# Performance work log

Hardware: AMD Instinct MI355X
Metric: run time of the kernel (lower is better)

Reference implementation:

```python
import jax, jax.numpy as jnp
import numpy as np

G, W, H1, H2, H3 = 512, 64, 128, 128, 64
B = 1024

def setup_inputs() -> dict:
    key = jax.random.key(0)
    k0, k1, k2, k3 = jax.random.split(key, 4)
    inputs = jax.random.normal(k0, (B, G * W), dtype=jnp.float32)
    # Glorot-uniform-like scaled init for stacked per-SKU weights
    def glorot(k, shape):
        fan_in, fan_out = shape[-2], shape[-1]
        lim = jnp.sqrt(6.0 / (fan_in + fan_out)).astype(jnp.float32)
        return jax.random.uniform(k, shape, jnp.float32, -lim, lim)
    W1 = glorot(k1, (G, W, H1))
    W2 = glorot(k2, (G, H1, H2))
    W3 = glorot(k3, (G, H2, H3))
    return {"inputs": inputs, "W1": W1, "W2": W2, "W3": W3}

def reference(inputs, W1, W2, W3):
    # inputs: [B, G*W]  -> per-SKU blocks [B, G, W] (SKU-major slicing in original)
    b = inputs.shape[0]
    x = inputs.reshape(b, G, W)
    # Grouped (batched-over-SKU) GEMM + relu per layer; no dropout (training=None)
    x = jax.nn.relu(jnp.einsum('bgw,gwh->bgh', x, W1))  # [B, G, H1]
    x = jax.nn.relu(jnp.einsum('bgh,ghk->bgk', x, W2))  # [B, G, H2]
    x = jax.nn.relu(jnp.einsum('bgk,gko->bgo', x, W3))  # [B, G, H3]
    # concat of per-SKU outputs along axis 1 == SKU-major reshape
    return x.reshape(b, G * H3)
```

## Files before the change

### kernel.cpp

```cpp
#include <hip/hip_runtime.h>

#define NG  512
#define WIN 64
#define NH1 128
#define NH2 128
#define NH3 64
#define NBB 1024
#define GW  (NG*WIN)
#define GH3 (NG*NH3)

typedef __attribute__((ext_vector_type(8))) short bf16x8;
typedef __attribute__((ext_vector_type(4))) float f32x4;
typedef __attribute__((ext_vector_type(4))) unsigned int u32x4;

union frag_u { u32x4 u; bf16x8 h; };

__device__ __forceinline__ unsigned pk2bf(float a, float b) {
  unsigned ua = __builtin_bit_cast(unsigned, a);
  unsigned ub = __builtin_bit_cast(unsigned, b);
  ua += 0x7fffu + ((ua >> 16) & 1u);
  ub += 0x7fffu + ((ub >> 16) & 1u);
  return (ua >> 16) | (ub & 0xffff0000u);
}

__device__ __forceinline__ void permswap(unsigned &e, unsigned &o) {
  asm volatile("s_nop 1\n\t"
               "v_permlane32_swap_b32 %0, %1\n\t"
               "s_nop 1\n\t"
               "v_permlane16_swap_b32 %0, %1\n\t"
               "s_nop 1"
               : "+v"(e), "+v"(o));
}

template<int K, int H>
__device__ __forceinline__ void stage_frag(const float* __restrict__ gsrc,
                                           char* ldsBase, int tid) {
  constexpr int KC = K / 32;
  constexpr int NELEM = (K / 8) * H;
  #pragma unroll
  for (int lin = tid; lin < NELEM; lin += 512) {
    const int h  = lin & (H - 1);
    const int kb = lin / H;
    const float* p = gsrc + h + (size_t)(8 * kb) * H;
    unsigned w0 = pk2bf(p[0 * H], p[1 * H]);
    unsigned w1 = pk2bf(p[2 * H], p[3 * H]);
    unsigned w2 = pk2bf(p[4 * H], p[5 * H]);
    unsigned w3 = pk2bf(p[6 * H], p[7 * H]);
    const int mt = h >> 4, bl = h & 15, kc = kb >> 2, bq = kb & 3;
    const int byteoff = ((mt * KC + kc) * 64 + bq * 16 + bl) * 16;
    *(u32x4*)(ldsBase + byteoff) = (u32x4){w0, w1, w2, w3};
  }
}

__device__ __forceinline__ void mk_bfrag(const f32x4* acc, frag_u* bf) {
  #pragma unroll
  for (int kc = 0; kc < 4; ++kc) {
    f32x4 e = acc[2 * kc], o = acc[2 * kc + 1];
    unsigned E0 = pk2bf(fmaxf(e[0], 0.f), fmaxf(e[1], 0.f));
    unsigned E1 = pk2bf(fmaxf(e[2], 0.f), fmaxf(e[3], 0.f));
    unsigned O0 = pk2bf(fmaxf(o[0], 0.f), fmaxf(o[1], 0.f));
    unsigned O1 = pk2bf(fmaxf(o[2], 0.f), fmaxf(o[3], 0.f));
    permswap(E0, O0);
    permswap(E1, O1);
    bf[kc].u = (u32x4){E0, E1, O0, O1};
  }
}

__device__ __forceinline__ void ld_b1(const float* px, frag_u* b1) {
  #pragma unroll
  for (int kc = 0; kc < 2; ++kc) {
    f32x4 lo = *(const f32x4*)(px + 32 * kc);
    f32x4 hi = *(const f32x4*)(px + 32 * kc + 4);
    b1[kc].u = (u32x4){pk2bf(lo[0], lo[1]), pk2bf(lo[2], lo[3]),
                       pk2bf(hi[0], hi[1]), pk2bf(hi[2], hi[3])};
  }
}

__global__ __launch_bounds__(512, 4)
void DeepBlockDense_kernel(const float* __restrict__ x,
                           const float* __restrict__ w1,
                           const float* __restrict__ w2,
                           const float* __restrict__ w3,
                           float* __restrict__ out) {
  __shared__ __align__(16) char smem[65536];
  const int g    = blockIdx.x;
  const int tid  = threadIdx.x;
  const int lane = tid & 63;
  const int wid  = tid >> 6;
  const int bq   = lane >> 4;
  const int bl   = lane & 15;

  stage_frag<64 , 128>(w1 + (size_t)g * (64 * 128) , smem        , tid);
  stage_frag<128, 128>(w2 + (size_t)g * (128 * 128), smem + 16384, tid);
  stage_frag<128, 64 >(w3 + (size_t)g * (128 * 64) , smem + 49152, tid);
  __syncthreads();

  const char* aBase = smem + lane * 16;

  #pragma unroll 1
  for (int t = 0; t < 4; ++t) {
    const size_t r0 = (size_t)(t * 256 + wid * 16 + bl);
    const size_t r1 = r0 + 128;

    frag_u b1a[2], b1b[2];
    ld_b1(x + r0 * GW + g * 64 + 8 * bq, b1a);
    ld_b1(x + r1 * GW + g * 64 + 8 * bq, b1b);

    f32x4 acc1a[8] = {}, acc1b[8] = {};
    #pragma unroll
    for (int mt = 0; mt < 8; ++mt) {
      #pragma unroll
      for (int kc = 0; kc < 2; ++kc) {
        frag_u a;
        a.u = *(const u32x4*)(aBase + 1024 * (mt * 2 + kc));
        acc1a[mt] = __builtin_amdgcn_mfma_f32_16x16x32_bf16(a.h, b1a[kc].h, acc1a[mt], 0, 0, 0);
        acc1b[mt] = __builtin_amdgcn_mfma_f32_16x16x32_bf16(a.h, b1b[kc].h, acc1b[mt], 0, 0, 0);
      }
    }

    frag_u b2a[4], b2b[4];
    mk_bfrag(acc1a, b2a);
    mk_bfrag(acc1b, b2b);

    f32x4 acc2a[8] = {}, acc2b[8] = {};
    #pragma unroll
    for (int mt = 0; mt < 8; ++mt) {
      #pragma unroll
      for (int kc = 0; kc < 4; ++kc) {
        frag_u a;
        a.u = *(const u32x4*)(aBase + 16384 + 1024 * (mt * 4 + kc));
        acc2a[mt] = __builtin_amdgcn_mfma_f32_16x16x32_bf16(a.h, b2a[kc].h, acc2a[mt], 0, 0, 0);
        acc2b[mt] = __builtin_amdgcn_mfma_f32_16x16x32_bf16(a.h, b2b[kc].h, acc2b[mt], 0, 0, 0);
      }
    }

    frag_u b3a[4], b3b[4];
    mk_bfrag(acc2a, b3a);
    mk_bfrag(acc2b, b3b);

    f32x4 acc3a[4] = {}, acc3b[4] = {};
    #pragma unroll
    for (int mt = 0; mt < 4; ++mt) {
      #pragma unroll
      for (int kc = 0; kc < 4; ++kc) {
        frag_u a;
        a.u = *(const u32x4*)(aBase + 49152 + 1024 * (mt * 4 + kc));
        acc3a[mt] = __builtin_amdgcn_mfma_f32_16x16x32_bf16(a.h, b3a[kc].h, acc3a[mt], 0, 0, 0);
        acc3b[mt] = __builtin_amdgcn_mfma_f32_16x16x32_bf16(a.h, b3b[kc].h, acc3b[mt], 0, 0, 0);
      }
    }

    float* po0 = out + r0 * GH3 + g * 64 + 4 * bq;
    float* po1 = out + r1 * GH3 + g * 64 + 4 * bq;
    #pragma unroll
    for (int mt = 0; mt < 4; ++mt) {
      f32x4 va = acc3a[mt], vb = acc3b[mt];
      va[0] = fmaxf(va[0], 0.f); va[1] = fmaxf(va[1], 0.f);
      va[2] = fmaxf(va[2], 0.f); va[3] = fmaxf(va[3], 0.f);
      vb[0] = fmaxf(vb[0], 0.f); vb[1] = fmaxf(vb[1], 0.f);
      vb[2] = fmaxf(vb[2], 0.f); vb[3] = fmaxf(vb[3], 0.f);
      *(f32x4*)(po0 + 16 * mt) = va;
      *(f32x4*)(po1 + 16 * mt) = vb;
    }
  }
}

extern "C" void kernel_launch(void* const* d_in, const int* in_sizes, int n_in,
                              void* d_out, int out_size, void* d_ws, size_t ws_size,
                              hipStream_t stream) {
  const float* x  = (const float*)d_in[0];
  const float* w1 = (const float*)d_in[1];
  const float* w2 = (const float*)d_in[2];
  const float* w3 = (const float*)d_in[3];
  float* out = (float*)d_out;
  (void)in_sizes; (void)n_in; (void)out_size; (void)d_ws; (void)ws_size;
  DeepBlockDense_kernel<<<dim3(NG), dim3(512), 0, stream>>>(x, w1, w2, w3, out);
}
```

Before: 87.54 us.

## Interleave layer GEMMs per output-tile pair and use hardware bf16 conversion

```diff
diff --git a/kernel.cpp b/kernel.cpp
--- a/kernel.cpp
+++ b/kernel.cpp
@@ -1,26 +1,21 @@
 #include <hip/hip_runtime.h>
 
 #define NG  512
-#define WIN 64
-#define NH1 128
-#define NH2 128
-#define NH3 64
-#define NBB 1024
-#define GW  (NG*WIN)
-#define GH3 (NG*NH3)
+#define GW  32768
+#define GH3 32768
 
 typedef __attribute__((ext_vector_type(8))) short bf16x8;
 typedef __attribute__((ext_vector_type(4))) float f32x4;
 typedef __attribute__((ext_vector_type(4))) unsigned int u32x4;
+typedef __attribute__((ext_vector_type(2))) __bf16 bf16x2;
 
 union frag_u { u32x4 u; bf16x8 h; };
 
-__device__ __forceinline__ unsigned pk2bf(float a, float b) {
-  unsigned ua = __builtin_bit_cast(unsigned, a);
-  unsigned ub = __builtin_bit_cast(unsigned, b);
-  ua += 0x7fffu + ((ua >> 16) & 1u);
-  ub += 0x7fffu + ((ub >> 16) & 1u);
-  return (ua >> 16) | (ub & 0xffff0000u);
+#define MFMA __builtin_amdgcn_mfma_f32_16x16x32_bf16
+
+__device__ __forceinline__ unsigned cvt2bf(float a, float b) {
+  bf16x2 v = {(__bf16)a, (__bf16)b};
+  return __builtin_bit_cast(unsigned, v);
 }
 
 __device__ __forceinline__ void permswap(unsigned &e, unsigned &o) {
@@ -30,6 +25,16 @@
                "v_permlane16_swap_b32 %0, %1\n\t"
                "s_nop 1"
                : "+v"(e), "+v"(o));
+}
+
+__device__ __forceinline__ void mk_bfrag1(f32x4 e, f32x4 o, frag_u &bf) {
+  unsigned E0 = cvt2bf(fmaxf(e[0], 0.f), fmaxf(e[1], 0.f));
+  unsigned E1 = cvt2bf(fmaxf(e[2], 0.f), fmaxf(e[3], 0.f));
+  unsigned O0 = cvt2bf(fmaxf(o[0], 0.f), fmaxf(o[1], 0.f));
+  unsigned O1 = cvt2bf(fmaxf(o[2], 0.f), fmaxf(o[3], 0.f));
+  permswap(E0, O0);
+  permswap(E1, O1);
+  bf.u = (u32x4){E0, E1, O0, O1};
 }
 
 template<int K, int H>
@@ -42,27 +47,13 @@
     const int h  = lin & (H - 1);
     const int kb = lin / H;
     const float* p = gsrc + h + (size_t)(8 * kb) * H;
-    unsigned w0 = pk2bf(p[0 * H], p[1 * H]);
-    unsigned w1 = pk2bf(p[2 * H], p[3 * H]);
-    unsigned w2 = pk2bf(p[4 * H], p[5 * H]);
-    unsigned w3 = pk2bf(p[6 * H], p[7 * H]);
+    unsigned w0 = cvt2bf(p[0 * H], p[1 * H]);
+    unsigned w1 = cvt2bf(p[2 * H], p[3 * H]);
+    unsigned w2 = cvt2bf(p[4 * H], p[5 * H]);
+    unsigned w3 = cvt2bf(p[6 * H], p[7 * H]);
     const int mt = h >> 4, bl = h & 15, kc = kb >> 2, bq = kb & 3;
     const int byteoff = ((mt * KC + kc) * 64 + bq * 16 + bl) * 16;
     *(u32x4*)(ldsBase + byteoff) = (u32x4){w0, w1, w2, w3};
-  }
-}
-
-__device__ __forceinline__ void mk_bfrag(const f32x4* acc, frag_u* bf) {
-  #pragma unroll
-  for (int kc = 0; kc < 4; ++kc) {
-    f32x4 e = acc[2 * kc], o = acc[2 * kc + 1];
-    unsigned E0 = pk2bf(fmaxf(e[0], 0.f), fmaxf(e[1], 0.f));
-    unsigned E1 = pk2bf(fmaxf(e[2], 0.f), fmaxf(e[3], 0.f));
-    unsigned O0 = pk2bf(fmaxf(o[0], 0.f), fmaxf(o[1], 0.f));
-    unsigned O1 = pk2bf(fmaxf(o[2], 0.f), fmaxf(o[3], 0.f));
-    permswap(E0, O0);
-    permswap(E1, O1);
-    bf[kc].u = (u32x4){E0, E1, O0, O1};
   }
 }
 
@@ -71,8 +62,8 @@
   for (int kc = 0; kc < 2; ++kc) {
     f32x4 lo = *(const f32x4*)(px + 32 * kc);
     f32x4 hi = *(const f32x4*)(px + 32 * kc + 4);
-    b1[kc].u = (u32x4){pk2bf(lo[0], lo[1]), pk2bf(lo[2], lo[3]),
-                       pk2bf(hi[0], hi[1]), pk2bf(hi[2], hi[3])};
+    b1[kc].u = (u32x4){cvt2bf(lo[0], lo[1]), cvt2bf(lo[2], lo[3]),
+                       cvt2bf(hi[0], hi[1]), cvt2bf(hi[2], hi[3])};
   }
 }
 
@@ -88,7 +79,6 @@
   const int lane = tid & 63;
   const int wid  = tid >> 6;
   const int bq   = lane >> 4;
-  const int bl   = lane & 15;
 
   stage_frag<64 , 128>(w1 + (size_t)g * (64 * 128) , smem        , tid);
   stage_frag<128, 128>(w2 + (size_t)g * (128 * 128), smem + 16384, tid);
@@ -99,54 +89,54 @@
 
   #pragma unroll 1
   for (int t = 0; t < 4; ++t) {
-    const size_t r0 = (size_t)(t * 256 + wid * 16 + bl);
+    const size_t r0 = (size_t)(t * 256 + wid * 16 + (lane & 15));
     const size_t r1 = r0 + 128;
 
     frag_u b1a[2], b1b[2];
     ld_b1(x + r0 * GW + g * 64 + 8 * bq, b1a);
     ld_b1(x + r1 * GW + g * 64 + 8 * bq, b1b);
 
-    f32x4 acc1a[8] = {}, acc1b[8] = {};
+    frag_u b2a[4], b2b[4];
     #pragma unroll
-    for (int mt = 0; mt < 8; ++mt) {
+    for (int pr = 0; pr < 4; ++pr) {
+      f32x4 ea = {}, oa = {}, eb = {}, ob = {};
       #pragma unroll
       for (int kc = 0; kc < 2; ++kc) {
-        frag_u a;
-        a.u = *(const u32x4*)(aBase + 1024 * (mt * 2 + kc));
-        acc1a[mt] = __builtin_amdgcn_mfma_f32_16x16x32_bf16(a.h, b1a[kc].h, acc1a[mt], 0, 0, 0);
-        acc1b[mt] = __builtin_amdgcn_mfma_f32_16x16x32_bf16(a.h, b1b[kc].h, acc1b[mt], 0, 0, 0);
+        frag_u ae, ao;
+        ae.u = *(const u32x4*)(aBase + 1024 * ((2 * pr    ) * 2 + kc));
+        ao.u = *(const u32x4*)(aBase + 1024 * ((2 * pr + 1) * 2 + kc));
+        ea = MFMA(ae.h, b1a[kc].h, ea, 0, 0, 0);
+        eb = MFMA(ae.h, b1b[kc].h, eb, 0, 0, 0);
+        oa = MFMA(ao.h, b1a[kc].h, oa, 0, 0, 0);
+        ob = MFMA(ao.h, b1b[kc].h, ob, 0, 0, 0);
       }
+      mk_bfrag1(ea, oa, b2a[pr]);
+      mk_bfrag1(eb, ob, b2b[pr]);
     }
-
-    frag_u b2a[4], b2b[4];
-    mk_bfrag(acc1a, b2a);
-    mk_bfrag(acc1b, b2b);
-
-    f32x4 acc2a[8] = {}, acc2b[8] = {};
-    #pragma unroll
-    for (int mt = 0; mt < 8; ++mt) {
-      #pragma unroll
-      for (int kc = 0; kc < 4; ++kc) {
-        frag_u a;
-        a.u = *(const u32x4*)(aBase + 16384 + 1024 * (mt * 4 + kc));
-        acc2a[mt] = __builtin_amdgcn_mfma_f32_16x16x32_bf16(a.h, b2a[kc].h, acc2a[mt], 0, 0, 0);
-        acc2b[mt] = __builtin_amdgcn_mfma_f32_16x16x32_bf16(a.h, b2b[kc].h, acc2b[mt], 0, 0, 0);
-      }
-    }
-
-    frag_u b3a[4], b3b[4];
-    mk_bfrag(acc2a, b3a);
-    mk_bfrag(acc2b, b3b);
 
     f32x4 acc3a[4] = {}, acc3b[4] = {};
     #pragma unroll
-    for (int mt = 0; mt < 4; ++mt) {
+    for (int pr = 0; pr < 4; ++pr) {
+      f32x4 ea = {}, oa = {}, eb = {}, ob = {};
       #pragma unroll
       for (int kc = 0; kc < 4; ++kc) {
+        frag_u ae, ao;
+        ae.u = *(const u32x4*)(aBase + 16384 + 1024 * ((2 * pr    ) * 4 + kc));
+        ao.u = *(const u32x4*)(aBase + 16384 + 1024 * ((2 * pr + 1) * 4 + kc));
+        ea = MFMA(ae.h, b2a[kc].h, ea, 0, 0, 0);
+        eb = MFMA(ae.h, b2b[kc].h, eb, 0, 0, 0);
+        oa = MFMA(ao.h, b2a[kc].h, oa, 0, 0, 0);
+        ob = MFMA(ao.h, b2b[kc].h, ob, 0, 0, 0);
+      }
+      frag_u b3a, b3b;
+      mk_bfrag1(ea, oa, b3a);
+      mk_bfrag1(eb, ob, b3b);
+      #pragma unroll
+      for (int mt = 0; mt < 4; ++mt) {
         frag_u a;
-        a.u = *(const u32x4*)(aBase + 49152 + 1024 * (mt * 4 + kc));
-        acc3a[mt] = __builtin_amdgcn_mfma_f32_16x16x32_bf16(a.h, b3a[kc].h, acc3a[mt], 0, 0, 0);
-        acc3b[mt] = __builtin_amdgcn_mfma_f32_16x16x32_bf16(a.h, b3b[kc].h, acc3b[mt], 0, 0, 0);
+        a.u = *(const u32x4*)(aBase + 49152 + 1024 * (mt * 4 + pr));
+        acc3a[mt] = MFMA(a.h, b3a.h, acc3a[mt], 0, 0, 0);
+        acc3b[mt] = MFMA(a.h, b3b.h, acc3b[mt], 0, 0, 0);
       }
     }
 
```

After: 85.33 us. 1.03x faster.
